# Kernel tuning notes

Measured on AMD Instinct MI355X. Metric: run time of the kernel, lower is better.

## Reference

```python
import jax, jax.numpy as jnp
import numpy as np

B, N, DIM, H = 4, 1024, 384, 12
EPS = 1e-6


def setup_inputs() -> dict:
    key = jax.random.key(0)
    ks = jax.random.split(key, 5)
    return {
        "x": jax.random.normal(ks[0], (B, N, DIM), dtype=jnp.float32),
        "w_qkv": jax.random.normal(ks[1], (DIM, 3 * DIM), dtype=jnp.float32) * 0.05,
        "w_out": jax.random.normal(ks[2], (DIM, DIM), dtype=jnp.float32) * 0.05,
        "b_out": jax.random.normal(ks[3], (DIM,), dtype=jnp.float32) * 0.05,
        "toeplitz_w": jax.random.normal(ks[4], (2 * N - 1,), dtype=jnp.float32),
    }


def reference(x, w_qkv, w_out, b_out, toeplitz_w):
    b, n, c = x.shape
    d = c // H
    qkv = x @ w_qkv                                   # [B,N,3C]
    q, k, v = jnp.split(qkv, 3, axis=-1)
    def heads(t):
        return t.reshape(b, n, H, d).transpose(0, 2, 1, 3)  # [B,H,N,d]
    q, k, v = heads(q), heads(k), heads(v)
    q = jax.nn.relu(q) + EPS
    k = jax.nn.relu(k) + EPS
    # outer product kv signal: [B,H,N,d,d]
    kv = k[..., :, None] * v[..., None, :]
    kv_flat = kv.reshape(b * H, n, d * d)
    k_flat = k.reshape(b * H, n, d)
    combined = jnp.concatenate([kv_flat, k_flat], axis=-1)   # [BH,N,d^2+d]
    fft_len = 2 * n
    sig_f = jnp.fft.rfft(combined, n=fft_len, axis=1)        # [BH,N+1,d^2+d] complex
    w_pad = jnp.zeros(fft_len, dtype=x.dtype).at[: 2 * n - 1].set(toeplitz_w)
    w_rolled = jnp.roll(w_pad, -(n - 1))
    w_f = jnp.fft.rfft(w_rolled, n=fft_len)                  # [N+1]
    out_f = sig_f * w_f[None, :, None]
    out_t = jnp.fft.irfft(out_f, n=fft_len, axis=1)[:, :n, :]  # [BH,N,d^2+d]
    kv_conv = out_t[:, :, : d * d].reshape(b, H, n, d, d)
    k_conv = out_t[:, :, d * d:].reshape(b, H, n, d)
    num = jnp.einsum('bhnd,bhndc->bhnc', q, kv_conv)
    den = jnp.einsum('bhnd,bhnd->bhn', q, k_conv)[..., None] + EPS
    out = (num / den).transpose(0, 2, 1, 3).reshape(b, n, c)
    return out @ w_out.T + b_out
```

## Files before the change

kernel.cpp:

```cpp
#include <hip/hip_runtime.h>

#define EPS 1e-6f


__global__ __launch_bounds__(256) void qkv_gemm(const float* __restrict__ x,
                                                const float* __restrict__ w,
                                                float* __restrict__ qw,
                                                float* __restrict__ kw,
                                                float* __restrict__ vw) {
    __shared__ float As[32][68];
    __shared__ float Bs[32][68];
    const int t = threadIdx.x;
    const int m0 = blockIdx.y * 64;
    const int c0 = blockIdx.x * 64;
    const int tx = t & 15, ty = t >> 4;

    float acc[4][4];
#pragma unroll
    for (int i = 0; i < 4; i++)
#pragma unroll
        for (int j = 0; j < 4; j++) acc[i][j] = 0.f;

    for (int k0 = 0; k0 < 384; k0 += 32) {
        __syncthreads();
#pragma unroll
        for (int l = 0; l < 2; l++) {
            int idx = t * 2 + l;
            int r = idx >> 3, c4 = (idx & 7) * 4;
            float4 a = *(const float4*)(x + (size_t)(m0 + r) * 384 + k0 + c4);
            As[c4 + 0][r] = a.x;
            As[c4 + 1][r] = a.y;
            As[c4 + 2][r] = a.z;
            As[c4 + 3][r] = a.w;
        }
#pragma unroll
        for (int l = 0; l < 2; l++) {
            int idx = t * 2 + l;
            int kr = idx >> 4, cc = (idx & 15) * 4;
            *(float4*)&Bs[kr][cc] = *(const float4*)(w + (size_t)(k0 + kr) * 1152 + c0 + cc);
        }
        __syncthreads();
#pragma unroll
        for (int kk = 0; kk < 32; kk++) {
            float4 a = *(float4*)&As[kk][ty * 4];
            float4 bb = *(float4*)&Bs[kk][tx * 4];
            float av[4] = {a.x, a.y, a.z, a.w};
            float bv[4] = {bb.x, bb.y, bb.z, bb.w};
#pragma unroll
            for (int i = 0; i < 4; i++)
#pragma unroll
                for (int j = 0; j < 4; j++) acc[i][j] += av[i] * bv[j];
        }
    }
    const int sec = (c0 + tx * 4) / 384;
    float* dst = (sec == 0) ? qw : (sec == 1) ? kw : vw;
    const int cc0 = c0 + tx * 4 - sec * 384;
    const int h = cc0 >> 5, dd = cc0 & 31;
#pragma unroll
    for (int i = 0; i < 4; i++) {
        int row = m0 + ty * 4 + i;
        int b = row >> 10, n = row & 1023;
        float4 o;
        if (sec < 2) {
            o.x = fmaxf(acc[i][0], 0.f) + EPS;
            o.y = fmaxf(acc[i][1], 0.f) + EPS;
            o.z = fmaxf(acc[i][2], 0.f) + EPS;
            o.w = fmaxf(acc[i][3], 0.f) + EPS;
        } else {
            o = make_float4(acc[i][0], acc[i][1], acc[i][2], acc[i][3]);
        }
        *(float4*)(dst + (size_t)((b * 12 + h) * 1024 + n) * 32 + dd) = o;
    }
}

__global__ __launch_bounds__(256) void toep_attn(const float* __restrict__ q,
                                                 const float* __restrict__ k,
                                                 const float* __restrict__ v,
                                                 const float* __restrict__ tw,
                                                 float* __restrict__ op) {
    const int t = threadIdx.x;
    const int r = t & 63;
    const int wv = __builtin_amdgcn_readfirstlane(t >> 6);
    const int n0 = blockIdx.x * 64;
    const int bh = blockIdx.y;
    const int b = bh / 12, h = bh % 12;

    __shared__ float Tw[1088];
    __shared__ double red[64][33];

    const float* qb = q + (size_t)bh * 32768;
    const float* kb = k + (size_t)bh * 32768;
    const float* vb = v + (size_t)bh * 32768;

    for (int j = t; j < 1087; j += 256) Tw[j] = tw[n0 + j];

    float qr[32];
#pragma unroll
    for (int c = 0; c < 8; c++) {
        float4 f = *(const float4*)(qb + (size_t)(n0 + r) * 32 + c * 4);
        qr[c * 4 + 0] = f.x; qr[c * 4 + 1] = f.y;
        qr[c * 4 + 2] = f.z; qr[c * 4 + 3] = f.w;
    }
    __syncthreads();

    double num[32];
#pragma unroll
    for (int c = 0; c < 32; c++) num[c] = 0.0;
    double den = 0.0;

    for (int m = wv; m < 1024; m += 4) {
        const float* kr = kb + (size_t)m * 32;
        const float* vr = vb + (size_t)m * 32;
        float s = 0.f;
#pragma unroll
        for (int d = 0; d < 32; d++) s += qr[d] * kr[d];
        s *= Tw[r - m + 1023];
        double sd = (double)s;
        den += sd;
#pragma unroll
        for (int c = 0; c < 32; c++) num[c] += sd * (double)vr[c];
    }

    if (wv == 0) {
#pragma unroll
        for (int c = 0; c < 32; c++) red[r][c] = num[c];
        red[r][32] = den;
    }
    __syncthreads();
    if (wv == 1) {
#pragma unroll
        for (int c = 0; c < 32; c++) red[r][c] += num[c];
        red[r][32] += den;
    }
    __syncthreads();
    if (wv == 2) {
#pragma unroll
        for (int c = 0; c < 32; c++) red[r][c] += num[c];
        red[r][32] += den;
    }
    __syncthreads();
    if (wv == 3) {
#pragma unroll
        for (int c = 0; c < 32; c++) red[r][c] += num[c];
        red[r][32] += den;
    }
    __syncthreads();

    {
        double inv = 1.0 / (red[r][32] + (double)EPS);
        float* o = op + (size_t)(b * 1024 + n0 + r) * 384 + h * 32 + wv * 8;
        float4 o0, o1;
        o0.x = (float)(red[r][wv * 8 + 0] * inv);
        o0.y = (float)(red[r][wv * 8 + 1] * inv);
        o0.z = (float)(red[r][wv * 8 + 2] * inv);
        o0.w = (float)(red[r][wv * 8 + 3] * inv);
        o1.x = (float)(red[r][wv * 8 + 4] * inv);
        o1.y = (float)(red[r][wv * 8 + 5] * inv);
        o1.z = (float)(red[r][wv * 8 + 6] * inv);
        o1.w = (float)(red[r][wv * 8 + 7] * inv);
        *(float4*)o = o0;
        *(float4*)(o + 4) = o1;
    }
}

__global__ __launch_bounds__(256) void out_gemm(const float* __restrict__ a,
                                                const float* __restrict__ w,
                                                const float* __restrict__ bias,
                                                float* __restrict__ out) {
    __shared__ float As[32][68];
    __shared__ float Bs[32][68];
    const int t = threadIdx.x;
    const int m0 = blockIdx.y * 64;
    const int c0 = blockIdx.x * 64;
    const int tx = t & 15, ty = t >> 4;

    float acc[4][4];
#pragma unroll
    for (int i = 0; i < 4; i++)
#pragma unroll
        for (int j = 0; j < 4; j++) acc[i][j] = 0.f;

    for (int k0 = 0; k0 < 384; k0 += 32) {
        __syncthreads();
#pragma unroll
        for (int l = 0; l < 2; l++) {
            int idx = t * 2 + l;
            int r = idx >> 3, c4 = (idx & 7) * 4;
            float4 av = *(const float4*)(a + (size_t)(m0 + r) * 384 + k0 + c4);
            As[c4 + 0][r] = av.x;
            As[c4 + 1][r] = av.y;
            As[c4 + 2][r] = av.z;
            As[c4 + 3][r] = av.w;
        }
#pragma unroll
        for (int l = 0; l < 2; l++) {
            int idx = t * 2 + l;
            int r = idx >> 3, c4 = (idx & 7) * 4;
            float4 wv = *(const float4*)(w + (size_t)(c0 + r) * 384 + k0 + c4);
            Bs[c4 + 0][r] = wv.x;
            Bs[c4 + 1][r] = wv.y;
            Bs[c4 + 2][r] = wv.z;
            Bs[c4 + 3][r] = wv.w;
        }
        __syncthreads();
#pragma unroll
        for (int kk = 0; kk < 32; kk++) {
            float4 a4 = *(float4*)&As[kk][ty * 4];
            float4 b4 = *(float4*)&Bs[kk][tx * 4];
            float av[4] = {a4.x, a4.y, a4.z, a4.w};
            float bv[4] = {b4.x, b4.y, b4.z, b4.w};
#pragma unroll
            for (int i = 0; i < 4; i++)
#pragma unroll
                for (int j = 0; j < 4; j++) acc[i][j] += av[i] * bv[j];
        }
    }
    const int col = c0 + tx * 4;
    float4 bb = *(const float4*)(bias + col);
#pragma unroll
    for (int i = 0; i < 4; i++) {
        int row = m0 + ty * 4 + i;
        float4 o = {acc[i][0] + bb.x, acc[i][1] + bb.y,
                    acc[i][2] + bb.z, acc[i][3] + bb.w};
        *(float4*)(out + (size_t)row * 384 + col) = o;
    }
}

extern "C" void kernel_launch(void* const* d_in, const int* in_sizes, int n_in,
                              void* d_out, int out_size, void* d_ws, size_t ws_size,
                              hipStream_t stream) {
    const float* x     = (const float*)d_in[0];
    const float* w_qkv = (const float*)d_in[1];
    const float* w_out = (const float*)d_in[2];
    const float* b_out = (const float*)d_in[3];
    const float* tw    = (const float*)d_in[4];
    float* out = (float*)d_out;

    float* qw = (float*)d_ws;
    float* kw = qw + 1572864;
    float* vw = kw + 1572864;
    float* op = vw + 1572864;

    qkv_gemm<<<dim3(18, 64), 256, 0, stream>>>(x, w_qkv, qw, kw, vw);
    toep_attn<<<dim3(16, 48), 256, 0, stream>>>(qw, kw, vw, tw, op);
    out_gemm<<<dim3(6, 64), 256, 0, stream>>>(op, w_out, b_out, out);
}
```

Baseline: 338.3 us.

## Split Toeplitz attention key loop across eight waves, optionally store V as double

The attention kernel now runs 512 threads (eight waves), each striding over keys by 8, so the serial key loop per block is halved and occupancy per block rises. The output write is reorganised so each thread writes one float4 from the shared reduction buffer. When the workspace is large enough, the QKV GEMM stores V in double precision so the attention loop skips the float-to-double conversion, at the cost of twice the V memory traffic. The wave reduction uses more serialized barrier steps, and the double-precision loads may increase register and bandwidth pressure.

```diff
diff --git a/kernel.cpp b/kernel.cpp
--- a/kernel.cpp
+++ b/kernel.cpp
@@ -3,11 +3,13 @@
 #define EPS 1e-6f
 
 
+template <bool V64>
 __global__ __launch_bounds__(256) void qkv_gemm(const float* __restrict__ x,
                                                 const float* __restrict__ w,
                                                 float* __restrict__ qw,
                                                 float* __restrict__ kw,
-                                                float* __restrict__ vw) {
+                                                float* __restrict__ vwf,
+                                                double* __restrict__ vwd) {
     __shared__ float As[32][68];
     __shared__ float Bs[32][68];
     const int t = threadIdx.x;
@@ -53,29 +55,37 @@
         }
     }
     const int sec = (c0 + tx * 4) / 384;
-    float* dst = (sec == 0) ? qw : (sec == 1) ? kw : vw;
     const int cc0 = c0 + tx * 4 - sec * 384;
     const int h = cc0 >> 5, dd = cc0 & 31;
 #pragma unroll
     for (int i = 0; i < 4; i++) {
         int row = m0 + ty * 4 + i;
         int b = row >> 10, n = row & 1023;
-        float4 o;
+        size_t base = (size_t)((b * 12 + h) * 1024 + n) * 32 + dd;
         if (sec < 2) {
+            float* dst = (sec == 0) ? qw : kw;
+            float4 o;
             o.x = fmaxf(acc[i][0], 0.f) + EPS;
             o.y = fmaxf(acc[i][1], 0.f) + EPS;
             o.z = fmaxf(acc[i][2], 0.f) + EPS;
             o.w = fmaxf(acc[i][3], 0.f) + EPS;
+            *(float4*)(dst + base) = o;
+        } else if (V64) {
+            double2 d0 = {(double)acc[i][0], (double)acc[i][1]};
+            double2 d1 = {(double)acc[i][2], (double)acc[i][3]};
+            *(double2*)(vwd + base) = d0;
+            *(double2*)(vwd + base + 2) = d1;
         } else {
-            o = make_float4(acc[i][0], acc[i][1], acc[i][2], acc[i][3]);
-        }
-        *(float4*)(dst + (size_t)((b * 12 + h) * 1024 + n) * 32 + dd) = o;
-    }
-}
-
-__global__ __launch_bounds__(256) void toep_attn(const float* __restrict__ q,
+            float4 o = make_float4(acc[i][0], acc[i][1], acc[i][2], acc[i][3]);
+            *(float4*)(vwf + base) = o;
+        }
+    }
+}
+
+template <typename VT>
+__global__ __launch_bounds__(512) void toep_attn(const float* __restrict__ q,
                                                  const float* __restrict__ k,
-                                                 const float* __restrict__ v,
+                                                 const VT* __restrict__ v,
                                                  const float* __restrict__ tw,
                                                  float* __restrict__ op) {
     const int t = threadIdx.x;
@@ -90,9 +100,9 @@
 
     const float* qb = q + (size_t)bh * 32768;
     const float* kb = k + (size_t)bh * 32768;
-    const float* vb = v + (size_t)bh * 32768;
-
-    for (int j = t; j < 1087; j += 256) Tw[j] = tw[n0 + j];
+    const VT*    vb = v + (size_t)bh * 32768;
+
+    for (int j = t; j < 1087; j += 512) Tw[j] = tw[n0 + j];
 
     float qr[32];
 #pragma unroll
@@ -108,9 +118,9 @@
     for (int c = 0; c < 32; c++) num[c] = 0.0;
     double den = 0.0;
 
-    for (int m = wv; m < 1024; m += 4) {
+    for (int m = wv; m < 1024; m += 8) {
         const float* kr = kb + (size_t)m * 32;
-        const float* vr = vb + (size_t)m * 32;
+        const VT*    vr = vb + (size_t)m * 32;
         float s = 0.f;
 #pragma unroll
         for (int d = 0; d < 32; d++) s += qr[d] * kr[d];
@@ -127,39 +137,25 @@
         red[r][32] = den;
     }
     __syncthreads();
-    if (wv == 1) {
-#pragma unroll
-        for (int c = 0; c < 32; c++) red[r][c] += num[c];
-        red[r][32] += den;
-    }
-    __syncthreads();
-    if (wv == 2) {
-#pragma unroll
-        for (int c = 0; c < 32; c++) red[r][c] += num[c];
-        red[r][32] += den;
-    }
-    __syncthreads();
-    if (wv == 3) {
-#pragma unroll
-        for (int c = 0; c < 32; c++) red[r][c] += num[c];
-        red[r][32] += den;
-    }
-    __syncthreads();
+#pragma unroll 1
+    for (int ww = 1; ww < 8; ww++) {
+        if (wv == ww) {
+#pragma unroll
+            for (int c = 0; c < 32; c++) red[r][c] += num[c];
+            red[r][32] += den;
+        }
+        __syncthreads();
+    }
 
     {
-        double inv = 1.0 / (red[r][32] + (double)EPS);
-        float* o = op + (size_t)(b * 1024 + n0 + r) * 384 + h * 32 + wv * 8;
-        float4 o0, o1;
-        o0.x = (float)(red[r][wv * 8 + 0] * inv);
-        o0.y = (float)(red[r][wv * 8 + 1] * inv);
-        o0.z = (float)(red[r][wv * 8 + 2] * inv);
-        o0.w = (float)(red[r][wv * 8 + 3] * inv);
-        o1.x = (float)(red[r][wv * 8 + 4] * inv);
-        o1.y = (float)(red[r][wv * 8 + 5] * inv);
-        o1.z = (float)(red[r][wv * 8 + 6] * inv);
-        o1.w = (float)(red[r][wv * 8 + 7] * inv);
-        *(float4*)o = o0;
-        *(float4*)(o + 4) = o1;
+        int orow = t >> 3, cg = (t & 7) * 4;
+        double inv = 1.0 / (red[orow][32] + (double)EPS);
+        float4 o;
+        o.x = (float)(red[orow][cg + 0] * inv);
+        o.y = (float)(red[orow][cg + 1] * inv);
+        o.z = (float)(red[orow][cg + 2] * inv);
+        o.w = (float)(red[orow][cg + 3] * inv);
+        *(float4*)(op + (size_t)(b * 1024 + n0 + orow) * 384 + h * 32 + cg) = o;
     }
 }
 
@@ -236,12 +232,21 @@
     const float* tw    = (const float*)d_in[4];
     float* out = (float*)d_out;
 
-    float* qw = (float*)d_ws;
-    float* kw = qw + 1572864;
-    float* vw = kw + 1572864;
-    float* op = vw + 1572864;
-
-    qkv_gemm<<<dim3(18, 64), 256, 0, stream>>>(x, w_qkv, qw, kw, vw);
-    toep_attn<<<dim3(16, 48), 256, 0, stream>>>(qw, kw, vw, tw, op);
+    char* ws = (char*)d_ws;
+    float* qw = (float*)ws;
+    float* kw = (float*)(ws + 6291456);
+    float* op = (float*)(ws + 12582912);
+    const size_t V64_NEED = 18ull * 1024 * 1024 + 48ull * 1024 * 32 * sizeof(double);
+    bool v64 = ws_size >= V64_NEED;
+
+    if (v64) {
+        double* vw = (double*)(ws + 18874368);
+        qkv_gemm<true><<<dim3(18, 64), 256, 0, stream>>>(x, w_qkv, qw, kw, nullptr, vw);
+        toep_attn<double><<<dim3(16, 48), 512, 0, stream>>>(qw, kw, vw, tw, op);
+    } else {
+        float* vw = (float*)(ws + 18874368);
+        qkv_gemm<false><<<dim3(18, 64), 256, 0, stream>>>(x, w_qkv, qw, kw, vw, nullptr);
+        toep_attn<float><<<dim3(16, 48), 512, 0, stream>>>(qw, kw, vw, tw, op);
+    }
     out_gemm<<<dim3(6, 64), 256, 0, stream>>>(op, w_out, b_out, out);
 }
```

New measurement: 373.2 us. +10.3%, slower.
